# Optimization experiments

Measured on AMD Instinct MI355X. Metric: run time of the kernel, lower is better.

The kernel has to match this reference:

```python
import jax, jax.numpy as jnp
from jax import lax
import numpy as np

D_MODEL = 256
NQ = 256          # nqueries / npoint
RADIUS = 0.3
NSAMPLE = 16
EPS = 1e-5


def _conv1d(x, W, b):  # x: (B,C,N), W: (O,C)
    return jnp.einsum('bcn,oc->bon', x, W) + b[None, :, None]


def _bn1d(x, g, be):  # train-mode batchnorm over (B, N)
    m = x.mean(axis=(0, 2), keepdims=True)
    v = x.var(axis=(0, 2), keepdims=True)
    return g[None, :, None] * (x - m) * lax.rsqrt(v + EPS) + be[None, :, None]


def _bn2d(x, g, be):  # x: (B,C,Q,S)
    m = x.mean(axis=(0, 2, 3), keepdims=True)
    v = x.var(axis=(0, 2, 3), keepdims=True)
    return g[None, :, None, None] * (x - m) * lax.rsqrt(v + EPS) + be[None, :, None, None]


def _fps(xyz, nq):
    # sequential farthest point sampling, starts at index 0 (matches CUDA impl)
    B, N, _ = xyz.shape

    def step(carry, _):
        dist, far = carry
        centroid = jnp.take_along_axis(xyz, far[:, None, None], axis=1)  # (B,1,3)
        d = jnp.sum((xyz - centroid) ** 2, axis=-1)                      # (B,N)
        dist = jnp.minimum(dist, d)
        nxt = jnp.argmax(dist, axis=-1).astype(jnp.int32)
        return (dist, nxt), far

    init = (jnp.full((B, N), 1e10, xyz.dtype), jnp.zeros((B,), jnp.int32))
    _, inds = lax.scan(step, init, None, length=nq)
    return inds.T  # (B,nq)


def _ball_query(query_xyz, xyz, radius, nsample):
    # query_xyz: (B,Q,3), xyz: (B,N,3) -> idx (B,Q,nsample) int32
    N = xyz.shape[1]
    d2 = jnp.sum((query_xyz[:, :, None, :] - xyz[:, None, :, :]) ** 2, axis=-1)  # (B,Q,N)
    within = d2 < radius * radius
    scores = jnp.where(within, jnp.arange(N, dtype=jnp.int32), jnp.int32(N))
    neg_top, _ = lax.top_k(-scores, nsample)          # nsample smallest scores, in order
    idx = -neg_top                                    # (B,Q,nsample)
    cnt = within.sum(axis=-1)                         # (B,Q)
    first = jnp.where(cnt > 0, idx[..., 0], 0)        # fill value (first neighbor, else 0)
    valid = jnp.arange(nsample) < cnt[..., None]
    return jnp.where(valid, idx, first[..., None])


def setup_inputs() -> dict:
    key = jax.random.key(0)
    ks = jax.random.split(key, 32)
    B, N, C = 16, 4096, D_MODEL
    s = 0.02
    inp = {
        'encode_xyz': jax.random.uniform(ks[0], (B, N, 3), jnp.float32),
        'encode_features': jax.random.normal(ks[1], (B, C, N), jnp.float32),
        # FFN_vote: conv1 -> bn -> relu -> conv2 -> bn -> relu -> conv3
        'W1': jax.random.normal(ks[2], (C, C), jnp.float32) * s,
        'b1': jnp.zeros((C,), jnp.float32),
        'g1': jnp.ones((C,), jnp.float32),
        'be1': jnp.zeros((C,), jnp.float32),
        'W2': jax.random.normal(ks[3], (C, C), jnp.float32) * s,
        'b2': jnp.zeros((C,), jnp.float32),
        'g2': jnp.ones((C,), jnp.float32),
        'be2': jnp.zeros((C,), jnp.float32),
        'W3': jax.random.normal(ks[4], (3 + C, C), jnp.float32) * s,
        'b3': jnp.zeros((3 + C,), jnp.float32),
        # SA module shared MLP (conv2d 1x1): (C+3)->C->C->C, each with BN2d
        'mW1': jax.random.normal(ks[5], (C, C + 3), jnp.float32) * s,
        'mb1': jnp.zeros((C,), jnp.float32),
        'mg1': jnp.ones((C,), jnp.float32),
        'mbe1': jnp.zeros((C,), jnp.float32),
        'mW2': jax.random.normal(ks[6], (C, C), jnp.float32) * s,
        'mb2': jnp.zeros((C,), jnp.float32),
        'mg2': jnp.ones((C,), jnp.float32),
        'mbe2': jnp.zeros((C,), jnp.float32),
        'mW3': jax.random.normal(ks[7], (C, C), jnp.float32) * s,
        'mb3': jnp.zeros((C,), jnp.float32),
        'mg3': jnp.ones((C,), jnp.float32),
        'mbe3': jnp.zeros((C,), jnp.float32),
    }
    return inp


def reference(encode_xyz, encode_features, W1, b1, g1, be1, W2, b2, g2, be2, W3, b3,
              mW1, mb1, mg1, mbe1, mW2, mb2, mg2, mbe2, mW3, mb3, mg3, mbe3):
    B, N, _ = encode_xyz.shape

    # FFN_vote
    h = jax.nn.relu(_bn1d(_conv1d(encode_features, W1, b1), g1, be1))
    h = jax.nn.relu(_bn1d(_conv1d(h, W2, b2), g2, be2))
    out = _conv1d(h, W3, b3)                      # (B, 3+C, N)

    coord_shift = jnp.clip(jax.nn.sigmoid(out[:, :3, :]), 0.1, 0.9)
    vote_xyz = encode_xyz + coord_shift.transpose(0, 2, 1) - 0.5   # (B,N,3)

    feat = encode_features + out[:, 3:, :]
    feat = feat / jnp.linalg.norm(feat, axis=1, keepdims=True)     # L2 normalize over C

    sample_inds = _fps(encode_xyz, NQ)                             # (B,NQ) int32

    # SA module: gather new centers from vote_xyz at FPS inds
    query_xyz = jnp.take_along_axis(vote_xyz, sample_inds[:, :, None], axis=1)  # (B,NQ,3)

    idx = _ball_query(query_xyz, vote_xyz, RADIUS, NSAMPLE)        # (B,NQ,NS)
    bidx = jnp.arange(B)[:, None, None]
    grouped_xyz = (vote_xyz[bidx, idx] - query_xyz[:, :, None, :]) / RADIUS  # (B,NQ,NS,3)
    grouped_feat = feat.transpose(0, 2, 1)[bidx, idx]                         # (B,NQ,NS,C)
    g = jnp.concatenate([grouped_xyz, grouped_feat], axis=-1)                 # (B,NQ,NS,3+C)
    g = g.transpose(0, 3, 1, 2)                                               # (B,3+C,NQ,NS)

    g = jax.nn.relu(_bn2d(jnp.einsum('bcqs,oc->boqs', g, mW1) + mb1[None, :, None, None], mg1, mbe1))
    g = jax.nn.relu(_bn2d(jnp.einsum('bcqs,oc->boqs', g, mW2) + mb2[None, :, None, None], mg2, mbe2))
    g = jax.nn.relu(_bn2d(jnp.einsum('bcqs,oc->boqs', g, mW3) + mb3[None, :, None, None], mg3, mbe3))
    query_features = jnp.max(g, axis=-1)                                      # (B,C,NQ)

    return vote_xyz, encode_xyz, sample_inds, query_xyz, query_features
```

## Files before the change

### kernel.cpp

```cpp
#include <hip/hip_runtime.h>
#include <math.h>

#define NPT 4096
#define NB 16

typedef short v8s __attribute__((ext_vector_type(8)));
typedef float v4f __attribute__((ext_vector_type(4)));

__device__ __forceinline__ float dist2e(float x, float y, float z,
                                        float cx, float cy, float cz) {
    float dx = __fsub_rn(x, cx), dy = __fsub_rn(y, cy), dz = __fsub_rn(z, cz);
    return __fadd_rn(__fadd_rn(__fmul_rn(dx, dx), __fmul_rn(dy, dy)), __fmul_rn(dz, dz));
}

__device__ __forceinline__ unsigned long long packdi(float v, int n) {
    return ((unsigned long long)__float_as_uint(v) << 32) |
           (unsigned long long)(0xFFFFFFFFu - (unsigned)n);
}

__device__ __forceinline__ unsigned short f2bf(float f) {
    unsigned u = __float_as_uint(f);
    u = u + 0x7FFFu + ((u >> 16) & 1u);
    return (unsigned short)(u >> 16);
}

__device__ __forceinline__ unsigned pk2(float a, float b) {
    unsigned r;
    asm("v_cvt_pk_bf16_f32 %0, %1, %2" : "=v"(r) : "v"(a), "v"(b));
    return r;
}

__device__ __forceinline__ uint2 split2(float a, float b) {
    unsigned h = pk2(a, b);
    float ra = __uint_as_float(h << 16);
    float rb = __uint_as_float(h & 0xFFFF0000u);
    unsigned l = pk2(a - ra, b - rb);
    return make_uint2(h, l);
}

__device__ __forceinline__ void bn8(v4f* xv, const float* __restrict__ scl,
                                    const float* __restrict__ sft, int base) {
    const v4f s0 = *(const v4f*)(scl + base);
    const v4f s1 = *(const v4f*)(scl + base + 4);
    const v4f f0 = *(const v4f*)(sft + base);
    const v4f f1 = *(const v4f*)(sft + base + 4);
    #pragma unroll
    for (int i = 0; i < 8; ++i) {
        const float si = (i < 4) ? s0[i] : s1[i - 4];
        const float fi = (i < 4) ? f0[i] : f1[i - 4];
        #pragma unroll
        for (int j = 0; j < 4; ++j)
            xv[i][j] = fmaxf(fmaf(xv[i][j], si, fi), 0.f);
    }
}

template <int CTRL>
__device__ __forceinline__ float dpp_maxf(float v) {
    int o = __builtin_amdgcn_update_dpp(__float_as_int(v), __float_as_int(v),
                                        CTRL, 0xF, 0xF, false);
    return fmaxf(v, __int_as_float(o));
}
template <int CTRL>
__device__ __forceinline__ unsigned dpp_maxu(unsigned v) {
    unsigned o = (unsigned)__builtin_amdgcn_update_dpp((int)v, (int)v,
                                                       CTRL, 0xF, 0xF, false);
    return v > o ? v : o;
}

__device__ void fps_seg(const float* __restrict__ xyz, int b, int it0, int it1,
                        int* __restrict__ inds_i, float* __restrict__ inds_f,
                        float* __restrict__ dws, int* __restrict__ farws,
                        char* scr) {
    unsigned long long (*s_red)[4] = (unsigned long long (*)[4])scr;
    const int t = threadIdx.x;
    const int lane = t & 63, wid = t >> 6;
    const float* pb = xyz + (size_t)b * NPT * 3;
    float px[16], py[16], pz[16], d[16];
    #pragma unroll
    for (int j = 0; j < 16; ++j) {
        int p = j * 256 + t;
        px[j] = pb[p * 3 + 0];
        py[j] = pb[p * 3 + 1];
        pz[j] = pb[p * 3 + 2];
    }
    int far;
    if (it0 == 0) {
        #pragma unroll
        for (int j = 0; j < 16; ++j) d[j] = 1e10f;
        far = 0;
    } else {
        #pragma unroll
        for (int j = 0; j < 16; ++j) d[j] = dws[b * 4096 + j * 256 + t];
        far = farws[b];
    }
    for (int it = it0; it < it1; ++it) {
        const int par = it & 1;
        if (t == 0) { inds_i[it] = far; inds_f[it] = (float)far; }
        const float cx = pb[far * 3 + 0];
        const float cy = pb[far * 3 + 1];
        const float cz = pb[far * 3 + 2];
        d[0] = fminf(d[0], dist2e(px[0], py[0], pz[0], cx, cy, cz));
        unsigned long long best = packdi(d[0], t);
        #pragma unroll
        for (int j = 1; j < 16; ++j) {
            d[j] = fminf(d[j], dist2e(px[j], py[j], pz[j], cx, cy, cz));
            unsigned long long c = packdi(d[j], j * 256 + t);
            if (c > best) best = c;
        }
        const unsigned hi = (unsigned)(best >> 32);
        const unsigned lo = (unsigned)(best & 0xFFFFFFFFull);
        float m = __uint_as_float(hi);
        m = dpp_maxf<0x111>(m);
        m = dpp_maxf<0x112>(m);
        m = dpp_maxf<0x114>(m);
        m = dpp_maxf<0x118>(m);
        m = dpp_maxf<0x142>(m);
        m = dpp_maxf<0x143>(m);
        const unsigned mbits = (unsigned)__builtin_amdgcn_readlane(__float_as_int(m), 63);
        unsigned cand = (hi == mbits) ? lo : 0u;
        cand = dpp_maxu<0x111>(cand);
        cand = dpp_maxu<0x112>(cand);
        cand = dpp_maxu<0x114>(cand);
        cand = dpp_maxu<0x118>(cand);
        cand = dpp_maxu<0x142>(cand);
        cand = dpp_maxu<0x143>(cand);
        const unsigned wlo = (unsigned)__builtin_amdgcn_readlane((int)cand, 63);
        if (lane == 0)
            s_red[par][wid] = ((unsigned long long)mbits << 32) | (unsigned long long)wlo;
        __syncthreads();
        unsigned long long mm = s_red[par][0];
        if (s_red[par][1] > mm) mm = s_red[par][1];
        if (s_red[par][2] > mm) mm = s_red[par][2];
        if (s_red[par][3] > mm) mm = s_red[par][3];
        far = (int)(0xFFFFFFFFu - (unsigned)(mm & 0xFFFFFFFFull));
    }
    if (it1 < 256) {
        #pragma unroll
        for (int j = 0; j < 16; ++j) dws[b * 4096 + j * 256 + t] = d[j];
        if (t == 0) farws[b] = far;
    }
}

template <bool PRE_BN, bool STATS>
__global__ __launch_bounds__(256, 4)
void fgemm_k(const float* __restrict__ X,
             const unsigned short* __restrict__ Wh,
             const unsigned short* __restrict__ Wl,
             const float* __restrict__ bias,
             const float* __restrict__ scl, const float* __restrict__ sft,
             float* __restrict__ Y,
             float* __restrict__ psum, float* __restrict__ psqr,
             const float* __restrict__ xyz, int* __restrict__ sinds,
             float* __restrict__ inds_f, float* __restrict__ fpsd,
             int* __restrict__ fpsfar, int it0, int it1) {
    __shared__ __align__(16) unsigned short sBh[128 * 64];
    __shared__ __align__(16) unsigned short sBl[128 * 64];
    if (blockIdx.x < 16) {
        fps_seg(xyz, blockIdx.x, it0, it1, sinds + blockIdx.x * 256,
                inds_f + blockIdx.x * 256, fpsd, fpsfar, (char*)sBh);
        return;
    }
    int idx = blockIdx.x - 16;
    idx = (idx & 7) * 128 + (idx >> 3);
    const int b = idx >> 6, rem = idx & 63;
    const int nt = rem >> 1;
    const int n0 = nt * 128, o0 = (rem & 1) * 128;
    const int t = threadIdx.x;
    const int w = t >> 6, lane = t & 63;
    const int wm = (w >> 1) * 64, wn = (w & 1) * 64;
    const int lr = lane & 15, lk = lane >> 4;
    char* cBh = (char*)sBh;
    char* cBl = (char*)sBl;

    v4f acc[4][4];
    v4f zz = {0.f, 0.f, 0.f, 0.f};
    #pragma unroll
    for (int i = 0; i < 4; ++i)
        #pragma unroll
        for (int j = 0; j < 4; ++j) acc[i][j] = zz;

    const size_t aoff = (size_t)(o0 + wm + lr) * 256 + lk * 8;
    const unsigned short* pah = Wh + aoff;
    const unsigned short* pal = Wl + aoff;

    const int cblk = t >> 5, nq = t & 31;
    const float* xb = X + ((size_t)b * 256 + cblk * 8) * 4096 + n0 + nq * 4;

    v4f cur[8];
    #pragma unroll
    for (int i = 0; i < 8; ++i)
        cur[i] = *(const v4f*)(xb + (size_t)i * 4096);
    if (PRE_BN) bn8(cur, scl, sft, cblk * 8);

    #pragma unroll
    for (int ks = 0; ks < 4; ++ks) {
        const int k0 = ks * 64;
        __syncthreads();
        #pragma unroll
        for (int j = 0; j < 4; ++j) {
            const int n = nq * 4 + j;
            uint2 p0 = split2(cur[0][j], cur[1][j]);
            uint2 p1 = split2(cur[2][j], cur[3][j]);
            uint2 p2 = split2(cur[4][j], cur[5][j]);
            uint2 p3 = split2(cur[6][j], cur[7][j]);
            uint4 hh, ll;
            hh.x = p0.x; hh.y = p1.x; hh.z = p2.x; hh.w = p3.x;
            ll.x = p0.y; ll.y = p1.y; ll.z = p2.y; ll.w = p3.y;
            const int ad = n * 128 + ((cblk * 16) ^ ((n & 7) << 4));
            *(uint4*)(cBh + ad) = hh;
            *(uint4*)(cBl + ad) = ll;
        }
        __syncthreads();
        if (ks < 3) {
            #pragma unroll
            for (int i = 0; i < 8; ++i)
                cur[i] = *(const v4f*)(xb + (size_t)(k0 + 64 + i) * 4096);
            if (PRE_BN) bn8(cur, scl, sft, k0 + 64 + cblk * 8);
        }
        #pragma unroll
        for (int kb = 0; kb < 2; ++kb) {
            const int koff = kb * 64 + lk * 16;
            const int ka = k0 + kb * 32;
            v8s ahf[4], alf[4], bhf[4], blf[4];
            #pragma unroll
            for (int f = 0; f < 4; ++f) {
                ahf[f] = *(const v8s*)(pah + (size_t)f * 4096 + ka);
                alf[f] = *(const v8s*)(pal + (size_t)f * 4096 + ka);
                const int rn = wn + f * 16 + lr;
                const int bm = rn * 128 + (koff ^ ((rn & 7) << 4));
                bhf[f] = *(const v8s*)(cBh + bm);
                blf[f] = *(const v8s*)(cBl + bm);
            }
            #pragma unroll
            for (int fm = 0; fm < 4; ++fm)
                #pragma unroll
                for (int fn = 0; fn < 4; ++fn) {
                    acc[fm][fn] = __builtin_amdgcn_mfma_f32_16x16x32_bf16(
                        ahf[fm], bhf[fn], acc[fm][fn], 0, 0, 0);
                    acc[fm][fn] = __builtin_amdgcn_mfma_f32_16x16x32_bf16(
                        ahf[fm], blf[fn], acc[fm][fn], 0, 0, 0);
                    acc[fm][fn] = __builtin_amdgcn_mfma_f32_16x16x32_bf16(
                        alf[fm], bhf[fn], acc[fm][fn], 0, 0, 0);
                }
        }
    }

    float* Yb = Y + (size_t)b * 256 * 4096;
    const int gnt = b * 32 + nt;
    #pragma unroll
    for (int fm = 0; fm < 4; ++fm) {
        const int obase = o0 + wm + fm * 16 + lk * 4;
        float bv[4];
        #pragma unroll
        for (int j = 0; j < 4; ++j) bv[j] = bias[obase + j];
        float ssr[4] = {0.f, 0.f, 0.f, 0.f}, qqr[4] = {0.f, 0.f, 0.f, 0.f};
        #pragma unroll
        for (int fn = 0; fn < 4; ++fn) {
            const int gn = n0 + wn + fn * 16 + lr;
            #pragma unroll
            for (int j = 0; j < 4; ++j) {
                const float yv = acc[fm][fn][j] + bv[j];
                Yb[(size_t)(obase + j) * 4096 + gn] = yv;
                ssr[j] += yv; qqr[j] += yv * yv;
            }
        }
        if (STATS) {
            #pragma unroll
            for (int j = 0; j < 4; ++j) {
                #pragma unroll
                for (int off = 1; off < 16; off <<= 1) {
                    ssr[j] += __shfl_xor(ssr[j], off, 64);
                    qqr[j] += __shfl_xor(qqr[j], off, 64);
                }
            }
            if (lr == 0) {
                const int col = gnt * 2 + (w & 1);
                #pragma unroll
                for (int j = 0; j < 4; ++j) {
                    psum[(size_t)(obase + j) * 1024 + col] = ssr[j];
                    psqr[(size_t)(obase + j) * 1024 + col] = qqr[j];
                }
            }
        }
    }
}

__global__ __launch_bounds__(256)
void prepw_k(const float* __restrict__ W1, const float* __restrict__ W2,
             const float* __restrict__ W3, unsigned short* __restrict__ h1,
             unsigned short* __restrict__ l1, unsigned short* __restrict__ h2,
             unsigned short* __restrict__ l2, unsigned short* __restrict__ h3,
             unsigned short* __restrict__ l3) {
    const int o = blockIdx.x & 255, which = blockIdx.x >> 8, t = threadIdx.x;
    float v;
    unsigned short* ph;
    unsigned short* pl;
    if (which == 0) { v = W1[(size_t)o * 256 + t]; ph = h1; pl = l1; }
    else if (which == 1) { v = W2[(size_t)o * 256 + t]; ph = h2; pl = l2; }
    else { v = W3[(size_t)(o + 3) * 256 + t]; ph = h3; pl = l3; }
    unsigned short hu = f2bf(v);
    float rv = v - __uint_as_float((unsigned)hu << 16);
    ph[o * 256 + t] = hu;
    pl[o * 256 + t] = f2bf(rv);
}

__global__ __launch_bounds__(64)
void fin_k(const float* __restrict__ psum, const float* __restrict__ psqr,
           const float* __restrict__ g, const float* __restrict__ be,
           float* __restrict__ scl, float* __restrict__ sft, int npart) {
    const int c = blockIdx.x, t = threadIdx.x;
    const float4* ps = (const float4*)(psum + (size_t)c * 1024);
    const float4* pq = (const float4*)(psqr + (size_t)c * 1024);
    float s = 0.f, q = 0.f;
    for (int r = t; r < (npart >> 2); r += 64) {
        float4 a = ps[r]; s += a.x + a.y + a.z + a.w;
        float4 b2 = pq[r]; q += b2.x + b2.y + b2.z + b2.w;
    }
    #pragma unroll
    for (int sh = 32; sh; sh >>= 1) {
        s += __shfl_down(s, (unsigned)sh, 64);
        q += __shfl_down(q, (unsigned)sh, 64);
    }
    if (t == 0) {
        float mean = s * (1.f / 65536.f);
        float var = q * (1.f / 65536.f) - mean * mean;
        float sc = g[c] / sqrtf(var + 1e-5f);
        scl[c] = sc;
        sft[c] = be[c] - mean * sc;
    }
}

__global__ __launch_bounds__(256)
void prep_k(const float* __restrict__ mW1, const float* __restrict__ mW2,
            const float* __restrict__ mW3, unsigned short* __restrict__ W1p,
            unsigned short* __restrict__ W2p, unsigned short* __restrict__ W3p) {
    const int o = blockIdx.x & 255, which = blockIdx.x >> 8, t = threadIdx.x;
    if (which == 0) {
        W1p[o * 320 + t] = f2bf(mW1[o * 259 + 3 + t]);
        if (t < 64) {
            float v = (t < 3) ? mW1[o * 259 + t] : 0.f;
            W1p[o * 320 + 256 + t] = f2bf(v);
        }
    } else if (which == 1) {
        W2p[o * 256 + t] = f2bf(mW2[o * 256 + t]);
    } else {
        W3p[o * 256 + t] = f2bf(mW3[o * 256 + t]);
    }
}

__global__ __launch_bounds__(256)
void votefeat_k(const float* __restrict__ OUT, const float* __restrict__ Y2,
                const float* __restrict__ xyz, const float* __restrict__ feats,
                const float* __restrict__ scl2, const float* __restrict__ sft2,
                const float* __restrict__ W3, const float* __restrict__ b3,
                float* __restrict__ vote_out, float* __restrict__ xyz_out,
                unsigned short* __restrict__ featT,
                int* __restrict__ sinds, float* __restrict__ inds_f,
                float* __restrict__ fpsd, int* __restrict__ fpsfar,
                int it0, int it1) {
    __shared__ float tile[32 * 257];
    __shared__ float ssb[32 * 9];
    __shared__ float rn[32];
    __shared__ float sW3[768];
    __shared__ float dred[3][8][33];
    if (blockIdx.x < 16) {
        fps_seg(xyz, blockIdx.x, it0, it1, sinds + blockIdx.x * 256,
                inds_f + blockIdx.x * 256, fpsd, fpsfar, (char*)tile);
        return;
    }
    const int blk = blockIdx.x - 16;
    const int b = blk >> 7, n0 = (blk & 127) * 32;
    const int t = threadIdx.x;
    const int nl = t & 31, co = t >> 5;
    const float* Ob = OUT + (size_t)b * 256 * NPT;
    const float* Yb = Y2 + (size_t)b * 256 * NPT;
    #pragma unroll
    for (int r = 0; r < 3; ++r) sW3[r * 256 + t] = W3[r * 256 + t];
    __syncthreads();
    float ss = 0.f, d0 = 0.f, d1 = 0.f, d2 = 0.f;
    #pragma unroll 4
    for (int ci = 0; ci < 32; ++ci) {
        const int c = ci * 8 + co;
        const size_t coff = (size_t)c * NPT + n0 + nl;
        float v = feats[(size_t)b * 256 * NPT + coff] + Ob[coff];
        tile[nl * 257 + c] = v;
        ss += v * v;
        float h = fmaxf(fmaf(Yb[coff], scl2[c], sft2[c]), 0.f);
        d0 = fmaf(h, sW3[c], d0);
        d1 = fmaf(h, sW3[256 + c], d1);
        d2 = fmaf(h, sW3[512 + c], d2);
    }
    ssb[nl * 9 + co] = ss;
    dred[0][co][nl] = d0;
    dred[1][co][nl] = d1;
    dred[2][co][nl] = d2;
    __syncthreads();
    if (t < 32) {
        float s = 0.f;
        #pragma unroll
        for (int j = 0; j < 8; ++j) s += ssb[t * 9 + j];
        rn[t] = 1.0f / sqrtf(s);
    }
    __syncthreads();
    for (int p = 0; p < 32; ++p)
        featT[((size_t)b * NPT + n0 + p) * 256 + t] = f2bf(tile[p * 257 + t] * rn[p]);
    if (t < 96) {
        const int r = t >> 5, p = t & 31;
        float d = b3[r];
        #pragma unroll
        for (int j = 0; j < 8; ++j) d += dred[r][j][p];
        float sig = 1.f / (1.f + expf(-d));
        sig = fminf(fmaxf(sig, 0.1f), 0.9f);
        const size_t gi = ((size_t)b * NPT + n0 + p) * 3 + r;
        const float e = xyz[gi];
        vote_out[gi] = e + sig - 0.5f;
        xyz_out[gi] = e;
    }
}

__global__ __launch_bounds__(64)
void bq_k(const float* __restrict__ vote, const int* __restrict__ sinds,
          float* __restrict__ qxyz_out, int* __restrict__ idx_out) {
    const int bq = blockIdx.x;
    const int b = bq >> 8;
    const int lane = threadIdx.x;
    __shared__ int s_idx[16];
    const int si = sinds[bq];
    const float* vb = vote + (size_t)b * NPT * 3;
    const float qx = vb[si * 3 + 0], qy = vb[si * 3 + 1], qz = vb[si * 3 + 2];
    if (lane < 3) qxyz_out[bq * 3 + lane] = vb[si * 3 + lane];
    int cnt = 0;
    for (int cb = 0; cb < 64 && cnt < 16; ++cb) {
        int n = cb * 64 + lane;
        float x = vb[n * 3], y = vb[n * 3 + 1], z = vb[n * 3 + 2];
        float d2 = dist2e(x, y, z, qx, qy, qz);
        unsigned long long m = __ballot(d2 < 0.09f);
        while (m && cnt < 16) {
            int bit = __builtin_ctzll(m);
            s_idx[cnt] = cb * 64 + bit;
            ++cnt;
            m &= m - 1;
        }
    }
    __syncthreads();
    if (lane < 16) {
        int v = (lane < cnt) ? s_idx[lane] : (cnt > 0 ? s_idx[0] : 0);
        idx_out[bq * 16 + lane] = v;
    }
}

__global__ __launch_bounds__(256)
void group_k(const unsigned short* __restrict__ featT, const float* __restrict__ vote,
             const float* __restrict__ qxyz, const int* __restrict__ idxs,
             unsigned short* __restrict__ Gt) {
    const int bq = blockIdx.x;
    const int b = bq >> 8, q = bq & 255;
    const int t = threadIdx.x;
    __shared__ int s_i[16];
    __shared__ float s_q[3];
    if (t < 16) s_i[t] = idxs[bq * 16 + t];
    if (t < 3) s_q[t] = qxyz[bq * 3 + t];
    __syncthreads();
    const int s = t >> 4, part = t & 15;
    const int i = s_i[s];
    const size_t nrow = (size_t)b * 4096 + q * 16 + s;
    const uint4* src = (const uint4*)(featT + ((size_t)b * NPT + i) * 256 + part * 16);
    uint4* dst = (uint4*)(Gt + nrow * 320 + part * 16);
    dst[0] = src[0];
    dst[1] = src[1];
    for (int c = 259 + part; c < 320; c += 16) Gt[nrow * 320 + c] = 0;
    if (part < 3) {
        float v = (vote[((size_t)b * NPT + i) * 3 + part] - s_q[part]) * (1.f / 0.3f);
        Gt[nrow * 320 + 256 + part] = f2bf(v);
    }
}

__device__ __forceinline__ unsigned bnpair(unsigned u, float sl, float sh,
                                           float fl, float fh) {
    float lo = __uint_as_float(u << 16);
    float hi = __uint_as_float(u & 0xFFFF0000u);
    lo = fmaxf(fmaf(lo, sl, fl), 0.f);
    hi = fmaxf(fmaf(hi, sh, fh), 0.f);
    unsigned r;
    asm("v_cvt_pk_bf16_f32 %0, %1, %2" : "=v"(r) : "v"(lo), "v"(hi));
    return r;
}

template <int KPAD, bool BNSTAGE, bool EPIMAX>
__global__ __launch_bounds__(256, 2)
void mgemm_k(const unsigned short* __restrict__ Wb,
             const unsigned short* __restrict__ Xt,
             const float* __restrict__ bias,
             const float* __restrict__ scl, const float* __restrict__ sft,
             unsigned short* __restrict__ Yt, float* __restrict__ rmax,
             float* __restrict__ psum, float* __restrict__ psqr) {
    __shared__ __align__(16) unsigned short sA[128 * 64];
    __shared__ __align__(16) unsigned short sB[128 * 64];
    char* cA = (char*)sA;
    char* cB = (char*)sB;
    const int t = threadIdx.x;
    const int n0 = blockIdx.x * 128, o0 = blockIdx.y * 128;
    const int w = t >> 6, lane = t & 63;
    const int wm = (w >> 1) * 64, wn = (w & 1) * 64;
    const int lr = lane & 15, lk = lane >> 4;

    v4f acc[4][4];
    v4f zz = {0.f, 0.f, 0.f, 0.f};
    #pragma unroll
    for (int i = 0; i < 4; ++i)
        #pragma unroll
        for (int j = 0; j < 4; ++j) acc[i][j] = zz;

    const int ra = t >> 1, kc = (t & 1) * 32;
    const unsigned short* asrc = Wb + (size_t)(o0 + ra) * KPAD + kc;
    const unsigned short* bsrc = Xt + (size_t)(n0 + ra) * KPAD + kc;
    constexpr int nk = KPAD / 64;

    uint4 av[4], bv[4];
    #pragma unroll
    for (int i = 0; i < 4; ++i) av[i] = *(const uint4*)(asrc + 8 * i);
    #pragma unroll
    for (int i = 0; i < 4; ++i) bv[i] = *(const uint4*)(bsrc + 8 * i);
    if constexpr (BNSTAGE) {
        #pragma unroll
        for (int i = 0; i < 4; ++i) {
            const int kk = kc + 8 * i;
            float4 s0 = *(const float4*)(scl + kk);
            float4 s1 = *(const float4*)(scl + kk + 4);
            float4 f0 = *(const float4*)(sft + kk);
            float4 f1 = *(const float4*)(sft + kk + 4);
            bv[i].x = bnpair(bv[i].x, s0.x, s0.y, f0.x, f0.y);
            bv[i].y = bnpair(bv[i].y, s0.z, s0.w, f0.z, f0.w);
            bv[i].z = bnpair(bv[i].z, s1.x, s1.y, f1.x, f1.y);
            bv[i].w = bnpair(bv[i].w, s1.z, s1.w, f1.z, f1.w);
        }
    }

    #pragma unroll
    for (int ks = 0; ks < nk; ++ks) {
        __syncthreads();
        #pragma unroll
        for (int i = 0; i < 4; ++i) {
            const int kb2 = (kc + 8 * i) * 2;
            *(uint4*)(cA + ra * 128 + (kb2 ^ ((ra & 7) << 4))) = av[i];
            *(uint4*)(cB + ra * 128 + (kb2 ^ ((ra & 7) << 4))) = bv[i];
        }
        __syncthreads();
        if (ks + 1 < nk) {
            const int k1 = (ks + 1) * 64;
            #pragma unroll
            for (int i = 0; i < 4; ++i) av[i] = *(const uint4*)(asrc + k1 + 8 * i);
            #pragma unroll
            for (int i = 0; i < 4; ++i) bv[i] = *(const uint4*)(bsrc + k1 + 8 * i);
            if constexpr (BNSTAGE) {
                #pragma unroll
                for (int i = 0; i < 4; ++i) {
                    const int kk = k1 + kc + 8 * i;
                    float4 s0 = *(const float4*)(scl + kk);
                    float4 s1 = *(const float4*)(scl + kk + 4);
                    float4 f0 = *(const float4*)(sft + kk);
                    float4 f1 = *(const float4*)(sft + kk + 4);
                    bv[i].x = bnpair(bv[i].x, s0.x, s0.y, f0.x, f0.y);
                    bv[i].y = bnpair(bv[i].y, s0.z, s0.w, f0.z, f0.w);
                    bv[i].z = bnpair(bv[i].z, s1.x, s1.y, f1.x, f1.y);
                    bv[i].w = bnpair(bv[i].w, s1.z, s1.w, f1.z, f1.w);
                }
            }
        }
        #pragma unroll
        for (int kb = 0; kb < 2; ++kb) {
            const int koff = (kb * 32 + lk * 8) * 2;
            v8s af[4], bf[4];
            #pragma unroll
            for (int f = 0; f < 4; ++f) {
                const int rm = wm + f * 16 + lr;
                af[f] = *(const v8s*)(cA + rm * 128 + (koff ^ ((rm & 7) << 4)));
                const int rn = wn + f * 16 + lr;
                bf[f] = *(const v8s*)(cB + rn * 128 + (koff ^ ((rn & 7) << 4)));
            }
            #pragma unroll
            for (int fm = 0; fm < 4; ++fm)
                #pragma unroll
                for (int fn = 0; fn < 4; ++fn)
                    acc[fm][fn] = __builtin_amdgcn_mfma_f32_16x16x32_bf16(
                        af[fm], bf[fn], acc[fm][fn], 0, 0, 0);
        }
    }

    const int bx = blockIdx.x;
    #pragma unroll
    for (int fm = 0; fm < 4; ++fm) {
        const int obase = o0 + wm + fm * 16 + lk * 4;
        const float4 bv4 = *(const float4*)(bias + obase);
        float s0 = 0.f, s1 = 0.f, s2 = 0.f, s3 = 0.f;
        float q0 = 0.f, q1 = 0.f, q2 = 0.f, q3 = 0.f;
        #pragma unroll
        for (int fn = 0; fn < 4; ++fn) {
            float y0 = acc[fm][fn][0] + bv4.x;
            float y1 = acc[fm][fn][1] + bv4.y;
            float y2 = acc[fm][fn][2] + bv4.z;
            float y3 = acc[fm][fn][3] + bv4.w;
            s0 += y0; s1 += y1; s2 += y2; s3 += y3;
            q0 += y0 * y0; q1 += y1 * y1; q2 += y2 * y2; q3 += y3 * y3;
            if constexpr (!EPIMAX) {
                unsigned p0, p1;
                asm("v_cvt_pk_bf16_f32 %0, %1, %2" : "=v"(p0) : "v"(y0), "v"(y1));
                asm("v_cvt_pk_bf16_f32 %0, %1, %2" : "=v"(p1) : "v"(y2), "v"(y3));
                const int gn = n0 + wn + fn * 16 + lr;
                *(uint2*)(Yt + (size_t)gn * 256 + obase) = make_uint2(p0, p1);
            } else {
                float m0 = y0, m1 = y1, m2 = y2, m3 = y3;
                #pragma unroll
                for (int off = 1; off < 16; off <<= 1) {
                    m0 = fmaxf(m0, __shfl_xor(m0, off, 64));
                    m1 = fmaxf(m1, __shfl_xor(m1, off, 64));
                    m2 = fmaxf(m2, __shfl_xor(m2, off, 64));
                    m3 = fmaxf(m3, __shfl_xor(m3, off, 64));
                }
                if (lr == 0) {
                    const int gq = (n0 + wn + fn * 16) >> 4;
                    const int bb = gq >> 8, qq = gq & 255;
                    float* rp = rmax + ((size_t)bb * 256 + obase) * 256 + qq;
                    rp[0] = m0; rp[256] = m1; rp[512] = m2; rp[768] = m3;
                }
            }
        }
        #pragma unroll
        for (int off = 1; off < 16; off <<= 1) {
            s0 += __shfl_xor(s0, off, 64); q0 += __shfl_xor(q0, off, 64);
            s1 += __shfl_xor(s1, off, 64); q1 += __shfl_xor(q1, off, 64);
            s2 += __shfl_xor(s2, off, 64); q2 += __shfl_xor(q2, off, 64);
            s3 += __shfl_xor(s3, off, 64); q3 += __shfl_xor(q3, off, 64);
        }
        if (lr == 0) {
            const int col = bx * 2 + (w & 1);
            psum[(size_t)(obase + 0) * 1024 + col] = s0;
            psum[(size_t)(obase + 1) * 1024 + col] = s1;
            psum[(size_t)(obase + 2) * 1024 + col] = s2;
            psum[(size_t)(obase + 3) * 1024 + col] = s3;
            psqr[(size_t)(obase + 0) * 1024 + col] = q0;
            psqr[(size_t)(obase + 1) * 1024 + col] = q1;
            psqr[(size_t)(obase + 2) * 1024 + col] = q2;
            psqr[(size_t)(obase + 3) * 1024 + col] = q3;
        }
    }
}

__global__ __launch_bounds__(256)
void qf_k(const float* __restrict__ rmax, const float* __restrict__ scl,
          const float* __restrict__ sft, float* __restrict__ out) {
    const int g = blockIdx.x * 256 + threadIdx.x;
    const int c = (g >> 8) & 255;
    out[g] = fmaxf(fmaf(rmax[g], scl[c], sft[c]), 0.f);
}

extern "C" void kernel_launch(void* const* d_in, const int* in_sizes, int n_in,
                              void* d_out, int out_size, void* d_ws, size_t ws_size,
                              hipStream_t stream) {
    const float* xyz   = (const float*)d_in[0];
    const float* feats = (const float*)d_in[1];
    const float* W1 = (const float*)d_in[2];
    const float* b1 = (const float*)d_in[3];
    const float* g1 = (const float*)d_in[4];
    const float* be1 = (const float*)d_in[5];
    const float* W2 = (const float*)d_in[6];
    const float* b2 = (const float*)d_in[7];
    const float* g2 = (const float*)d_in[8];
    const float* be2 = (const float*)d_in[9];
    const float* W3 = (const float*)d_in[10];
    const float* b3 = (const float*)d_in[11];
    const float* mW1 = (const float*)d_in[12];
    const float* mb1 = (const float*)d_in[13];
    const float* mg1 = (const float*)d_in[14];
    const float* mbe1 = (const float*)d_in[15];
    const float* mW2 = (const float*)d_in[16];
    const float* mb2 = (const float*)d_in[17];
    const float* mg2 = (const float*)d_in[18];
    const float* mbe2 = (const float*)d_in[19];
    const float* mW3 = (const float*)d_in[20];
    const float* mb3 = (const float*)d_in[21];
    const float* mg3 = (const float*)d_in[22];
    const float* mbe3 = (const float*)d_in[23];

    float* out_vote = (float*)d_out;
    float* out_xyz = out_vote + 196608;
    float* out_inds = out_xyz + 196608;
    float* out_q = out_inds + 4096;
    float* out_qf = out_q + 12288;

    float* ws = (float*)d_ws;
    float* A      = ws;
    float* Bb     = A + 16973824;
    float* Ft     = Bb + 16777216;
    float* rawmax = Ft + 8388608;
    float* psum   = rawmax + 1048576;
    float* psqr   = psum + 262144;
    float* st     = psqr + 262144;
    float* fpsd   = st + 2560;
    float* wbase  = fpsd + 65536;
    unsigned short* Wb1 = (unsigned short*)wbase;
    unsigned short* Wb2 = Wb1 + 81920;
    unsigned short* Wb3 = Wb2 + 65536;
    int* sinds  = (int*)(Wb3 + 65536);
    int* bidx   = sinds + 4096;
    int* fpsfar = bidx + 65536;

    unsigned short* Gt  = (unsigned short*)A;
    unsigned short* Y1t = (unsigned short*)Bb;
    unsigned short* featT = (unsigned short*)Ft;
    unsigned short* Y2t = (unsigned short*)Ft;

    unsigned short* Wf1h = (unsigned short*)rawmax;
    unsigned short* Wf1l = Wf1h + 65536;
    unsigned short* Wf2h = Wf1l + 65536;
    unsigned short* Wf2l = Wf2h + 65536;
    unsigned short* Wf3h = Wf2l + 65536;
    unsigned short* Wf3l = Wf3h + 65536;

    prep_k<<<768, 256, 0, stream>>>(mW1, mW2, mW3, Wb1, Wb2, Wb3);
    prepw_k<<<768, 256, 0, stream>>>(W1, W2, W3, Wf1h, Wf1l, Wf2h, Wf2l, Wf3h, Wf3l);

    fgemm_k<false, true><<<1040, 256, 0, stream>>>(
        feats, Wf1h, Wf1l, b1, nullptr, nullptr, A, psum, psqr,
        xyz, sinds, out_inds, fpsd, fpsfar, 0, 64);
    fin_k<<<256, 64, 0, stream>>>(psum, psqr, g1, be1, st + 0, st + 256, 1024);
    fgemm_k<true, true><<<1040, 256, 0, stream>>>(
        A, Wf2h, Wf2l, b2, st + 0, st + 256, Bb, psum, psqr,
        xyz, sinds, out_inds, fpsd, fpsfar, 64, 128);
    fin_k<<<256, 64, 0, stream>>>(psum, psqr, g2, be2, st + 512, st + 768, 1024);
    fgemm_k<true, false><<<1040, 256, 0, stream>>>(
        Bb, Wf3h, Wf3l, b3 + 3, st + 512, st + 768, A, nullptr, nullptr,
        xyz, sinds, out_inds, fpsd, fpsfar, 128, 192);

    votefeat_k<<<2064, 256, 0, stream>>>(A, Bb, xyz, feats, st + 512, st + 768,
                                         W3, b3, out_vote, out_xyz, featT,
                                         sinds, out_inds, fpsd, fpsfar, 192, 256);
    bq_k<<<4096, 64, 0, stream>>>(out_vote, sinds, out_q, bidx);
    group_k<<<4096, 256, 0, stream>>>(featT, out_vote, out_q, bidx, Gt);

    mgemm_k<320, false, false><<<dim3(512, 2), 256, 0, stream>>>(
        Wb1, Gt, mb1, nullptr, nullptr, Y1t, nullptr, psum, psqr);
    fin_k<<<256, 64, 0, stream>>>(psum, psqr, mg1, mbe1, st + 1024, st + 1280, 1024);
    mgemm_k<256, true, false><<<dim3(512, 2), 256, 0, stream>>>(
        Wb2, Y1t, mb2, st + 1024, st + 1280, Y2t, nullptr, psum, psqr);
    fin_k<<<256, 64, 0, stream>>>(psum, psqr, mg2, mbe2, st + 1536, st + 1792, 1024);
    mgemm_k<256, true, true><<<dim3(512, 2), 256, 0, stream>>>(
        Wb3, Y2t, mb3, st + 1536, st + 1792, nullptr, rawmax, psum, psqr);
    fin_k<<<256, 64, 0, stream>>>(psum, psqr, mg3, mbe3, st + 2048, st + 2304, 1024);
    qf_k<<<4096, 256, 0, stream>>>(rawmax, st + 2048, st + 2304, out_qf);
}
```

Measured before the change: 565.3 us.

## Fuse vote coordinate projection into third feature GEMM and raise mgemm occupancy

The 3-row coordinate projection (W3 rows 0-2 applied to BN+ReLU of Y2) moves out of votefeat_k and into the third fgemm_k. That GEMM already loads and normalizes the same activations, so it accumulates the dot products in registers for the o0==0 tiles, reduces them through shared memory and writes a small coordd buffer. votefeat_k therefore no longer rereads the full Y2 tensor. Separately, mgemm_k's launch bounds go from 2 to 3 blocks per CU, which may add register pressure or spills.

```diff
diff --git a/kernel.cpp b/kernel.cpp
--- a/kernel.cpp
+++ b/kernel.cpp
@@ -51,6 +51,20 @@
         #pragma unroll
         for (int j = 0; j < 4; ++j)
             xv[i][j] = fmaxf(fmaf(xv[i][j], si, fi), 0.f);
+    }
+}
+
+__device__ __forceinline__ void coord_acc(const v4f* cur, float (*ds)[4],
+                                          const float* __restrict__ w3, int base) {
+    #pragma unroll
+    for (int r = 0; r < 3; ++r) {
+        const float* p = w3 + r * 256 + base;
+        #pragma unroll
+        for (int i = 0; i < 8; ++i) {
+            const float wv = p[i];
+            #pragma unroll
+            for (int j = 0; j < 4; ++j) ds[r][j] = fmaf(cur[i][j], wv, ds[r][j]);
+        }
     }
 }
 
@@ -141,7 +155,7 @@
     }
 }
 
-template <bool PRE_BN, bool STATS>
+template <bool PRE_BN, bool STATS, bool COORD>
 __global__ __launch_bounds__(256, 4)
 void fgemm_k(const float* __restrict__ X,
              const unsigned short* __restrict__ Wh,
@@ -150,14 +164,16 @@
              const float* __restrict__ scl, const float* __restrict__ sft,
              float* __restrict__ Y,
              float* __restrict__ psum, float* __restrict__ psqr,
+             const float* __restrict__ W3c, float* __restrict__ coordd,
              const float* __restrict__ xyz, int* __restrict__ sinds,
              float* __restrict__ inds_f, float* __restrict__ fpsd,
              int* __restrict__ fpsfar, int it0, int it1) {
-    __shared__ __align__(16) unsigned short sBh[128 * 64];
-    __shared__ __align__(16) unsigned short sBl[128 * 64];
+    __shared__ __align__(16) char smem[32768];
+    char* cBh = smem;
+    char* cBl = smem + 16384;
     if (blockIdx.x < 16) {
         fps_seg(xyz, blockIdx.x, it0, it1, sinds + blockIdx.x * 256,
-                inds_f + blockIdx.x * 256, fpsd, fpsfar, (char*)sBh);
+                inds_f + blockIdx.x * 256, fpsd, fpsfar, smem);
         return;
     }
     int idx = blockIdx.x - 16;
@@ -169,8 +185,6 @@
     const int w = t >> 6, lane = t & 63;
     const int wm = (w >> 1) * 64, wn = (w & 1) * 64;
     const int lr = lane & 15, lk = lane >> 4;
-    char* cBh = (char*)sBh;
-    char* cBl = (char*)sBl;
 
     v4f acc[4][4];
     v4f zz = {0.f, 0.f, 0.f, 0.f};
@@ -178,6 +192,14 @@
     for (int i = 0; i < 4; ++i)
         #pragma unroll
         for (int j = 0; j < 4; ++j) acc[i][j] = zz;
+
+    float dsum[3][4];
+    if (COORD) {
+        #pragma unroll
+        for (int r = 0; r < 3; ++r)
+            #pragma unroll
+            for (int j = 0; j < 4; ++j) dsum[r][j] = 0.f;
+    }
 
     const size_t aoff = (size_t)(o0 + wm + lr) * 256 + lk * 8;
     const unsigned short* pah = Wh + aoff;
@@ -191,6 +213,7 @@
     for (int i = 0; i < 8; ++i)
         cur[i] = *(const v4f*)(xb + (size_t)i * 4096);
     if (PRE_BN) bn8(cur, scl, sft, cblk * 8);
+    if (COORD && o0 == 0) coord_acc(cur, dsum, W3c, cblk * 8);
 
     #pragma unroll
     for (int ks = 0; ks < 4; ++ks) {
@@ -216,6 +239,7 @@
             for (int i = 0; i < 8; ++i)
                 cur[i] = *(const v4f*)(xb + (size_t)(k0 + 64 + i) * 4096);
             if (PRE_BN) bn8(cur, scl, sft, k0 + 64 + cblk * 8);
+            if (COORD && o0 == 0) coord_acc(cur, dsum, W3c, k0 + 64 + cblk * 8);
         }
         #pragma unroll
         for (int kb = 0; kb < 2; ++kb) {
@@ -242,6 +266,29 @@
                     acc[fm][fn] = __builtin_amdgcn_mfma_f32_16x16x32_bf16(
                         alf[fm], bhf[fn], acc[fm][fn], 0, 0, 0);
                 }
+        }
+    }
+
+    if (COORD && o0 == 0) {
+        float* dred = (float*)smem;
+        __syncthreads();
+        #pragma unroll
+        for (int j = 0; j < 4; ++j) {
+            const int n = nq * 4 + j;
+            #pragma unroll
+            for (int r = 0; r < 3; ++r)
+                dred[(cblk * 128 + n) * 3 + r] = dsum[r][j];
+        }
+        __syncthreads();
+        if (t < 128) {
+            float a0 = 0.f, a1 = 0.f, a2 = 0.f;
+            #pragma unroll
+            for (int g = 0; g < 8; ++g) {
+                const float* p = &dred[(g * 128 + t) * 3];
+                a0 += p[0]; a1 += p[1]; a2 += p[2];
+            }
+            float* cp = coordd + ((size_t)b * 4096 + n0 + t) * 3;
+            cp[0] = a0; cp[1] = a1; cp[2] = a2;
         }
     }
 
@@ -349,10 +396,9 @@
 }
 
 __global__ __launch_bounds__(256)
-void votefeat_k(const float* __restrict__ OUT, const float* __restrict__ Y2,
-                const float* __restrict__ xyz, const float* __restrict__ feats,
-                const float* __restrict__ scl2, const float* __restrict__ sft2,
-                const float* __restrict__ W3, const float* __restrict__ b3,
+void votefeat_k(const float* __restrict__ OUT, const float* __restrict__ xyz,
+                const float* __restrict__ feats, const float* __restrict__ coordd,
+                const float* __restrict__ b3,
                 float* __restrict__ vote_out, float* __restrict__ xyz_out,
                 unsigned short* __restrict__ featT,
                 int* __restrict__ sinds, float* __restrict__ inds_f,
@@ -361,8 +407,6 @@
     __shared__ float tile[32 * 257];
     __shared__ float ssb[32 * 9];
     __shared__ float rn[32];
-    __shared__ float sW3[768];
-    __shared__ float dred[3][8][33];
     if (blockIdx.x < 16) {
         fps_seg(xyz, blockIdx.x, it0, it1, sinds + blockIdx.x * 256,
                 inds_f + blockIdx.x * 256, fpsd, fpsfar, (char*)tile);
@@ -373,11 +417,7 @@
     const int t = threadIdx.x;
     const int nl = t & 31, co = t >> 5;
     const float* Ob = OUT + (size_t)b * 256 * NPT;
-    const float* Yb = Y2 + (size_t)b * 256 * NPT;
-    #pragma unroll
-    for (int r = 0; r < 3; ++r) sW3[r * 256 + t] = W3[r * 256 + t];
-    __syncthreads();
-    float ss = 0.f, d0 = 0.f, d1 = 0.f, d2 = 0.f;
+    float ss = 0.f;
     #pragma unroll 4
     for (int ci = 0; ci < 32; ++ci) {
         const int c = ci * 8 + co;
@@ -385,15 +425,8 @@
         float v = feats[(size_t)b * 256 * NPT + coff] + Ob[coff];
         tile[nl * 257 + c] = v;
         ss += v * v;
-        float h = fmaxf(fmaf(Yb[coff], scl2[c], sft2[c]), 0.f);
-        d0 = fmaf(h, sW3[c], d0);
-        d1 = fmaf(h, sW3[256 + c], d1);
-        d2 = fmaf(h, sW3[512 + c], d2);
     }
     ssb[nl * 9 + co] = ss;
-    dred[0][co][nl] = d0;
-    dred[1][co][nl] = d1;
-    dred[2][co][nl] = d2;
     __syncthreads();
     if (t < 32) {
         float s = 0.f;
@@ -406,9 +439,7 @@
         featT[((size_t)b * NPT + n0 + p) * 256 + t] = f2bf(tile[p * 257 + t] * rn[p]);
     if (t < 96) {
         const int r = t >> 5, p = t & 31;
-        float d = b3[r];
-        #pragma unroll
-        for (int j = 0; j < 8; ++j) d += dred[r][j][p];
+        const float d = b3[r] + coordd[((size_t)b * 4096 + n0 + p) * 3 + r];
         float sig = 1.f / (1.f + expf(-d));
         sig = fminf(fmaxf(sig, 0.1f), 0.9f);
         const size_t gi = ((size_t)b * NPT + n0 + p) * 3 + r;
@@ -487,7 +518,7 @@
 }
 
 template <int KPAD, bool BNSTAGE, bool EPIMAX>
-__global__ __launch_bounds__(256, 2)
+__global__ __launch_bounds__(256, 3)
 void mgemm_k(const unsigned short* __restrict__ Wb,
              const unsigned short* __restrict__ Xt,
              const float* __restrict__ bias,
@@ -716,24 +747,25 @@
     unsigned short* Wf2l = Wf2h + 65536;
     unsigned short* Wf3h = Wf2l + 65536;
     unsigned short* Wf3l = Wf3h + 65536;
+    float* coordd = rawmax + 262144;
 
     prep_k<<<768, 256, 0, stream>>>(mW1, mW2, mW3, Wb1, Wb2, Wb3);
     prepw_k<<<768, 256, 0, stream>>>(W1, W2, W3, Wf1h, Wf1l, Wf2h, Wf2l, Wf3h, Wf3l);
 
-    fgemm_k<false, true><<<1040, 256, 0, stream>>>(
+    fgemm_k<false, true, false><<<1040, 256, 0, stream>>>(
         feats, Wf1h, Wf1l, b1, nullptr, nullptr, A, psum, psqr,
-        xyz, sinds, out_inds, fpsd, fpsfar, 0, 64);
+        nullptr, nullptr, xyz, sinds, out_inds, fpsd, fpsfar, 0, 64);
     fin_k<<<256, 64, 0, stream>>>(psum, psqr, g1, be1, st + 0, st + 256, 1024);
-    fgemm_k<true, true><<<1040, 256, 0, stream>>>(
+    fgemm_k<true, true, false><<<1040, 256, 0, stream>>>(
         A, Wf2h, Wf2l, b2, st + 0, st + 256, Bb, psum, psqr,
-        xyz, sinds, out_inds, fpsd, fpsfar, 64, 128);
+        nullptr, nullptr, xyz, sinds, out_inds, fpsd, fpsfar, 64, 128);
     fin_k<<<256, 64, 0, stream>>>(psum, psqr, g2, be2, st + 512, st + 768, 1024);
-    fgemm_k<true, false><<<1040, 256, 0, stream>>>(
+    fgemm_k<true, false, true><<<1040, 256, 0, stream>>>(
         Bb, Wf3h, Wf3l, b3 + 3, st + 512, st + 768, A, nullptr, nullptr,
-        xyz, sinds, out_inds, fpsd, fpsfar, 128, 192);
-
-    votefeat_k<<<2064, 256, 0, stream>>>(A, Bb, xyz, feats, st + 512, st + 768,
-                                         W3, b3, out_vote, out_xyz, featT,
+        W3, coordd, xyz, sinds, out_inds, fpsd, fpsfar, 128, 192);
+
+    votefeat_k<<<2064, 256, 0, stream>>>(A, xyz, feats, coordd, b3,
+                                         out_vote, out_xyz, featT,
                                          sinds, out_inds, fpsd, fpsfar, 192, 256);
     bq_k<<<4096, 64, 0, stream>>>(out_vote, sinds, out_q, bidx);
     group_k<<<4096, 256, 0, stream>>>(featT, out_vote, out_q, bidx, Gt);
```

New measurement: 680.8 us. 1.2x slower.
